# Performance work log

Measured on AMD Instinct MI355X. Metric: run time of the kernel, lower is better.

## Reference

```python
import jax, jax.numpy as jnp
import numpy as np

DIM = 512
HEADS = 8
SCALE = DIM ** (-0.5)  # scale_with_head=False


def setup_inputs() -> dict:
    key = jax.random.key(0)
    k1, k2, k3 = jax.random.split(key, 3)
    x = jax.random.normal(k1, (16, 1024, DIM), dtype=jnp.float32)
    w_qkv = jax.random.normal(k2, (DIM, 3 * DIM), dtype=jnp.float32) * (DIM ** -0.5)
    w_out = jax.random.normal(k3, (DIM, DIM), dtype=jnp.float32) * (DIM ** -0.5)
    b_out = jnp.zeros((DIM,), dtype=jnp.float32)
    return {"x": x, "w_qkv": w_qkv, "w_out": w_out, "b_out": b_out}


def reference(x, w_qkv, w_out, b_out):
    b, n, _ = x.shape
    h = HEADS
    qkv = x @ w_qkv  # [b, n, 3*dim]
    q, k, v = jnp.split(qkv, 3, axis=-1)
    # b n (h d) -> b h n d
    reshape = lambda t: t.reshape(b, n, h, -1).transpose(0, 2, 1, 3)
    q, k, v = reshape(q), reshape(k), reshape(v)
    dots = jnp.einsum('bhid,bhjd->bhij', q, k) * SCALE  # [b,h,n,n]
    attn = jax.nn.softmax(dots, axis=-1)
    out = jnp.einsum('bhij,bhjd->bhid', attn, v)
    out = out.transpose(0, 2, 1, 3).reshape(b, n, h * (DIM // h))  # b n (h d)
    return out @ w_out + b_out
```

## Files before the change

kernel.cpp:

```cpp
#include <hip/hip_runtime.h>
#include <math.h>


#define QSCALE_ 0.06376541773f
#define RESCALE_THR_ 8.0f

typedef float f32x4 __attribute__((ext_vector_type(4)));
typedef __bf16 bf16x8 __attribute__((ext_vector_type(8)));

static __device__ __forceinline__ ushort bf_bits(float f) {
    unsigned u = __builtin_bit_cast(unsigned, f);
    u += 0x7fffu + ((u >> 16) & 1u);
    return (ushort)(u >> 16);
}
static __device__ __forceinline__ unsigned cvt_pk_bf16(float lo, float hi) {
    unsigned d;
    asm("v_cvt_pk_bf16_f32 %0, %1, %2" : "=v"(d) : "v"(lo), "v"(hi));
    return d;
}

#define GLDS16(gsrc, ldst)                                                              \
    __builtin_amdgcn_global_load_lds((const __attribute__((address_space(1))) void*)(gsrc), \
                                     (__attribute__((address_space(3))) void*)(ldst), 16, 0, 0)

__global__ __launch_bounds__(256) void cast_bf16(const float* __restrict__ in,
                                                 ushort* __restrict__ out, int n4) {
    const int i = blockIdx.x * 256 + threadIdx.x;
    if (i >= n4) return;
    const float4 v = ((const float4*)in)[i];
    ushort4 o;
    o.x = bf_bits(v.x); o.y = bf_bits(v.y); o.z = bf_bits(v.z); o.w = bf_bits(v.w);
    ((ushort4*)out)[i] = o;
}

__global__ __launch_bounds__(256) void transpose_cast(const float* __restrict__ in,
                                                      ushort* __restrict__ out,
                                                      int K, int N, float scale, int scaleRows) {
    __shared__ float t[32][33];
    const int n0 = blockIdx.x * 32, k0 = blockIdx.y * 32;
    const int tx = threadIdx.x & 31, ty = threadIdx.x >> 5;
    for (int i = ty; i < 32; i += 8)
        t[i][tx] = in[(size_t)(k0 + i) * N + n0 + tx];
    __syncthreads();
    for (int i = ty; i < 32; i += 8) {
        const float s = (n0 + i < scaleRows) ? scale : 1.f;
        out[(size_t)(n0 + i) * K + k0 + tx] = bf_bits(t[tx][i] * s);
    }
}

__global__ __launch_bounds__(256) void gemm_bf16(const ushort* __restrict__ A,
                                                 const ushort* __restrict__ BT,
                                                 const float* __restrict__ bias,
                                                 float* __restrict__ C,
                                                 ushort* __restrict__ Cb,
                                                 ushort* __restrict__ VT,
                                                 int M, int N, int K) {
    __shared__ __align__(16) char lds[16384];
    const int tid = threadIdx.x;
    const int lane = tid & 63;
    const int w = tid >> 6;
    const int wr = w >> 1, wc = w & 1;
    const int fr = lane & 15;
    const int fg = lane >> 4;
    const int rowBase = blockIdx.y * 128;
    const int colBase = blockIdx.x * 128;

    f32x4 acc[4][4] = {};

    for (int k0 = 0; k0 < K; k0 += 32) {
#pragma unroll
        for (int r = 0; r < 2; ++r) {
            const unsigned boff = r * 4096u + w * 1024u + lane * 16u;
            const unsigned row = boff >> 6;
            const unsigned ke = (boff & 63u) >> 1;
            GLDS16(A + (size_t)(rowBase + row) * K + k0 + ke, lds + r * 4096 + w * 1024);
            GLDS16(BT + (size_t)(colBase + row) * K + k0 + ke, lds + 8192 + r * 4096 + w * 1024);
        }
        __syncthreads();

        bf16x8 a_frag[4], b_frag[4];
#pragma unroll
        for (int mi = 0; mi < 4; ++mi)
            a_frag[mi] = *(const bf16x8*)(lds + ((wr * 64 + mi * 16 + fr) * 64 + fg * 16));
#pragma unroll
        for (int ni = 0; ni < 4; ++ni)
            b_frag[ni] = *(const bf16x8*)(lds + 8192 + ((wc * 64 + ni * 16 + fr) * 64 + fg * 16));
#pragma unroll
        for (int mi = 0; mi < 4; ++mi)
#pragma unroll
            for (int ni = 0; ni < 4; ++ni)
                acc[mi][ni] = __builtin_amdgcn_mfma_f32_16x16x32_bf16(a_frag[mi], b_frag[ni],
                                                                      acc[mi][ni], 0, 0, 0);
        __syncthreads();
    }

#pragma unroll
    for (int ni = 0; ni < 4; ++ni) {
        const int col = colBase + wc * 64 + ni * 16 + fr;
        const float bv = bias ? bias[col] : 0.f;
#pragma unroll
        for (int mi = 0; mi < 4; ++mi) {
            const int row0 = rowBase + wr * 64 + mi * 16 + fg * 4;
            if (Cb) {
                if (VT && col >= 1024) {
                    const int hd = col - 1024;
                    const size_t vb = ((size_t)((row0 >> 10) * 8 + (hd >> 6)) * 64 + (hd & 63)) * 1024
                                      + (row0 & 1023);
                    ushort4 pk4;
                    pk4.x = bf_bits(acc[mi][ni][0]);
                    pk4.y = bf_bits(acc[mi][ni][1]);
                    pk4.z = bf_bits(acc[mi][ni][2]);
                    pk4.w = bf_bits(acc[mi][ni][3]);
                    *(ushort4*)(VT + vb) = pk4;
                } else {
#pragma unroll
                    for (int q = 0; q < 4; ++q)
                        Cb[(size_t)(row0 + q) * N + col] = bf_bits(acc[mi][ni][q]);
                }
            } else {
#pragma unroll
                for (int q = 0; q < 4; ++q)
                    C[(size_t)(row0 + q) * N + col] = acc[mi][ni][q] + bv;
            }
        }
    }
}

__global__ __launch_bounds__(256) void attn_mfma(const ushort* __restrict__ qkv,
                                                 const ushort* __restrict__ vT,
                                                 ushort* __restrict__ aoutb) {
    __shared__ __align__(16) char lds[40960];
    const int qt = blockIdx.x;
    const int bh = blockIdx.y;
    const int b = bh >> 3, h = bh & 7;
    const int tid = threadIdx.x;
    const int lane = tid & 63;
    const int w = tid >> 6;
    const int fr = lane & 15;
    const int fg = lane >> 4;

    const size_t nbase = (size_t)b * 1024;
    const int qrow0 = qt * 64;

    bf16x8 qf[2];
    {
        const size_t qa = (nbase + qrow0 + w * 16 + fr) * 1536 + h * 64;
        qf[0] = *(const bf16x8*)(qkv + qa + fg * 8);
        qf[1] = *(const bf16x8*)(qkv + qa + 32 + fg * 8);
    }

    const int srow = w * 16 + (lane >> 3);
    const int slot = lane & 7;
    auto stage = [&](int kt, int buf) {
        char* kd = lds + buf * 8192;
        char* vd = lds + 16384 + buf * 8192;
#pragma unroll
        for (int r = 0; r < 2; ++r) {
            const int row = srow + r * 8;
            const int sw = slot ^ (row & 7);
            GLDS16(qkv + (nbase + kt * 64 + row) * 1536 + 512 + h * 64 + sw * 8,
                   kd + (w * 2 + r) * 1024);
            GLDS16(vT + ((size_t)bh * 64 + row) * 1024 + kt * 64 + sw * 8,
                   vd + (w * 2 + r) * 1024);
        }
    };

    f32x4 o[4] = {};
    float mrow = -INFINITY, lrow = 0.f;

    stage(0, 0);
    __syncthreads();
    int cur = 0;
    char* const pbase = lds + 32768 + w * 2048;

    for (int kt = 0; kt < 16; ++kt) {
        if (kt < 15) stage(kt + 1, cur ^ 1);
        const char* kb = lds + cur * 8192;
        const char* vb = lds + 16384 + cur * 8192;

        f32x4 S[4];
#pragma unroll
        for (int jb = 0; jb < 4; ++jb) {
            f32x4 a = {};
#pragma unroll
            for (int s = 0; s < 2; ++s) {
                const int row = jb * 16 + fr;
                const int c = s * 64 + fg * 16;
                const bf16x8 kf = *(const bf16x8*)(kb + row * 128 + (c ^ ((row & 7) << 4)));
                a = __builtin_amdgcn_mfma_f32_16x16x32_bf16(kf, qf[s], a, 0, 0, 0);
            }
            S[jb] = a;
        }

        float tmax = -INFINITY;
#pragma unroll
        for (int jb = 0; jb < 4; ++jb)
#pragma unroll
            for (int r = 0; r < 4; ++r) tmax = fmaxf(tmax, S[jb][r]);
        tmax = fmaxf(tmax, __shfl_xor(tmax, 16));
        tmax = fmaxf(tmax, __shfl_xor(tmax, 32));

        if (!__all(tmax - mrow <= RESCALE_THR_)) {
            const float mnew = fmaxf(mrow, tmax);
            const float corr = __builtin_amdgcn_exp2f(mrow - mnew);
            mrow = mnew;
            lrow *= corr;
#pragma unroll
            for (int r = 0; r < 4; ++r) {
                const float cr = __shfl(corr, fg * 4 + r);
#pragma unroll
                for (int dvb = 0; dvb < 4; ++dvb) o[dvb][r] *= cr;
            }
        }

        float psum = 0.f;
#pragma unroll
        for (int jb = 0; jb < 4; ++jb)
#pragma unroll
            for (int r = 0; r < 4; ++r) {
                const float p = __builtin_amdgcn_exp2f(S[jb][r] - mrow);
                S[jb][r] = p;
                psum += p;
            }
        psum += __shfl_xor(psum, 16);
        psum += __shfl_xor(psum, 32);
        lrow += psum;

#pragma unroll
        for (int jb = 0; jb < 4; ++jb) {
            unsigned pk2[2];
            pk2[0] = cvt_pk_bf16(S[jb][0], S[jb][1]);
            pk2[1] = cvt_pk_bf16(S[jb][2], S[jb][3]);
            *(ulong1*)(pbase + fr * 128 + ((jb * 32 + fg * 8) ^ ((fr & 7) << 4))) =
                *(ulong1*)pk2;
        }

#pragma unroll
        for (int s = 0; s < 2; ++s) {
            const int pc = s * 64 + fg * 16;
            const bf16x8 pf = *(const bf16x8*)(pbase + fr * 128 + (pc ^ ((fr & 7) << 4)));
#pragma unroll
            for (int dvb = 0; dvb < 4; ++dvb) {
                const int vrow = dvb * 16 + fr;
                const bf16x8 vf = *(const bf16x8*)(vb + vrow * 128 + (pc ^ ((vrow & 7) << 4)));
                o[dvb] = __builtin_amdgcn_mfma_f32_16x16x32_bf16(pf, vf, o[dvb], 0, 0, 0);
            }
        }
        __syncthreads();
        cur ^= 1;
    }

#pragma unroll
    for (int r = 0; r < 4; ++r) {
        const float linv = 1.f / __shfl(lrow, fg * 4 + r);
        const size_t n = nbase + qrow0 + w * 16 + fg * 4 + r;
#pragma unroll
        for (int dvb = 0; dvb < 4; ++dvb)
            aoutb[n * 512 + h * 64 + dvb * 16 + fr] = bf_bits(o[dvb][r] * linv);
    }
}

extern "C" void kernel_launch(void* const* d_in, const int* in_sizes, int n_in,
                              void* d_out, int out_size, void* d_ws, size_t ws_size,
                              hipStream_t stream) {
    const float* x     = (const float*)d_in[0];
    const float* w_qkv = (const float*)d_in[1];
    const float* w_out = (const float*)d_in[2];
    const float* b_out = (const float*)d_in[3];
    float* out = (float*)d_out;

    char* ws = (char*)d_ws;
    ushort* qkvb  = (ushort*)ws;
    ushort* vT    = (ushort*)(ws + 50331648);
    ushort* xb    = (ushort*)(ws + 50331648 + 16777216);
    ushort* aoutb = xb;
    ushort* wqkvT = (ushort*)(ws + 50331648 + 33554432);
    ushort* woutT = (ushort*)(ws + 50331648 + 33554432 + 1572864);

    const dim3 blk(256);
    cast_bf16<<<dim3(8388608 / 4 / 256), blk, 0, stream>>>(x, xb, 8388608 / 4);
    transpose_cast<<<dim3(1536 / 32, 512 / 32), blk, 0, stream>>>(w_qkv, wqkvT, 512, 1536,
                                                                  QSCALE_, 512);
    transpose_cast<<<dim3(512 / 32, 512 / 32), blk, 0, stream>>>(w_out, woutT, 512, 512,
                                                                 1.f, 0);
    gemm_bf16<<<dim3(12, 128), blk, 0, stream>>>(xb, wqkvT, nullptr, nullptr, qkvb, vT,
                                                 16384, 1536, 512);
    attn_mfma<<<dim3(16, 128), blk, 0, stream>>>(qkvb, vT, aoutb);
    gemm_bf16<<<dim3(4, 128), blk, 0, stream>>>(aoutb, woutT, b_out, out, nullptr, nullptr,
                                                16384, 512, 512);
}
```

Before: 152.0 us.

## Fuse x cast into QKV GEMM and offload softmax row-sum to MFMA

Removes the standalone fp32-to-bf16 cast kernel for x. The QKV GEMM now loads fp32 rows directly, converts them in registers and writes them into a padded LDS tile. In the attention kernel, the row-sum of probabilities is computed by an MFMA against a ones vector instead of VALU adds and shuffles, and exp is fused into the bf16 packing. The kernel also adds s_setprio around MFMA blocks, uses 3-input max, and unrolls the K loop by two to fix buffer indices. The cost is that the fused GEMM re-reads fp32 x once per column block (12x) and swaps the async LDS loads for synchronous register loads.

```diff
diff --git a/kernel.cpp b/kernel.cpp
--- a/kernel.cpp
+++ b/kernel.cpp
@@ -18,20 +18,13 @@
     asm("v_cvt_pk_bf16_f32 %0, %1, %2" : "=v"(d) : "v"(lo), "v"(hi));
     return d;
 }
+static __device__ __forceinline__ float fmax3_(float a, float b, float c) {
+    return fmaxf(fmaxf(a, b), c);
+}
 
 #define GLDS16(gsrc, ldst)                                                              \
     __builtin_amdgcn_global_load_lds((const __attribute__((address_space(1))) void*)(gsrc), \
                                      (__attribute__((address_space(3))) void*)(ldst), 16, 0, 0)
-
-__global__ __launch_bounds__(256) void cast_bf16(const float* __restrict__ in,
-                                                 ushort* __restrict__ out, int n4) {
-    const int i = blockIdx.x * 256 + threadIdx.x;
-    if (i >= n4) return;
-    const float4 v = ((const float4*)in)[i];
-    ushort4 o;
-    o.x = bf_bits(v.x); o.y = bf_bits(v.y); o.z = bf_bits(v.z); o.w = bf_bits(v.w);
-    ((ushort4*)out)[i] = o;
-}
 
 __global__ __launch_bounds__(256) void transpose_cast(const float* __restrict__ in,
                                                       ushort* __restrict__ out,
@@ -48,14 +41,18 @@
     }
 }
 
-__global__ __launch_bounds__(256) void gemm_bf16(const ushort* __restrict__ A,
+template <bool FUSEA>
+__global__ __launch_bounds__(256) void gemm_bf16(const float* __restrict__ Af32,
+                                                 const ushort* __restrict__ A,
                                                  const ushort* __restrict__ BT,
                                                  const float* __restrict__ bias,
                                                  float* __restrict__ C,
                                                  ushort* __restrict__ Cb,
                                                  ushort* __restrict__ VT,
                                                  int M, int N, int K) {
-    __shared__ __align__(16) char lds[16384];
+    constexpr int ASTR = FUSEA ? 80 : 64;
+    constexpr int BOFF = FUSEA ? 10240 : 8192;
+    __shared__ __align__(16) char lds[BOFF + 8192];
     const int tid = threadIdx.x;
     const int lane = tid & 63;
     const int w = tid >> 6;
@@ -68,23 +65,47 @@
     f32x4 acc[4][4] = {};
 
     for (int k0 = 0; k0 < K; k0 += 32) {
-#pragma unroll
-        for (int r = 0; r < 2; ++r) {
-            const unsigned boff = r * 4096u + w * 1024u + lane * 16u;
-            const unsigned row = boff >> 6;
-            const unsigned ke = (boff & 63u) >> 1;
-            GLDS16(A + (size_t)(rowBase + row) * K + k0 + ke, lds + r * 4096 + w * 1024);
-            GLDS16(BT + (size_t)(colBase + row) * K + k0 + ke, lds + 8192 + r * 4096 + w * 1024);
+        if constexpr (FUSEA) {
+            const int ar = tid >> 1, kh = tid & 1;
+            const float* src = Af32 + (size_t)(rowBase + ar) * K + k0 + kh * 16;
+            const float4 v0 = ((const float4*)src)[0];
+            const float4 v1 = ((const float4*)src)[1];
+            const float4 v2 = ((const float4*)src)[2];
+            const float4 v3 = ((const float4*)src)[3];
+            uint4 lo, hi;
+            lo.x = cvt_pk_bf16(v0.x, v0.y); lo.y = cvt_pk_bf16(v0.z, v0.w);
+            lo.z = cvt_pk_bf16(v1.x, v1.y); lo.w = cvt_pk_bf16(v1.z, v1.w);
+            hi.x = cvt_pk_bf16(v2.x, v2.y); hi.y = cvt_pk_bf16(v2.z, v2.w);
+            hi.z = cvt_pk_bf16(v3.x, v3.y); hi.w = cvt_pk_bf16(v3.z, v3.w);
+            char* dst = lds + ar * 80 + kh * 32;
+            *(uint4*)dst = lo;
+            *(uint4*)(dst + 16) = hi;
+#pragma unroll
+            for (int r = 0; r < 2; ++r) {
+                const unsigned boff = r * 4096u + w * 1024u + lane * 16u;
+                const unsigned row = boff >> 6;
+                const unsigned ke = (boff & 63u) >> 1;
+                GLDS16(BT + (size_t)(colBase + row) * K + k0 + ke, lds + BOFF + r * 4096 + w * 1024);
+            }
+        } else {
+#pragma unroll
+            for (int r = 0; r < 2; ++r) {
+                const unsigned boff = r * 4096u + w * 1024u + lane * 16u;
+                const unsigned row = boff >> 6;
+                const unsigned ke = (boff & 63u) >> 1;
+                GLDS16(A + (size_t)(rowBase + row) * K + k0 + ke, lds + r * 4096 + w * 1024);
+                GLDS16(BT + (size_t)(colBase + row) * K + k0 + ke, lds + BOFF + r * 4096 + w * 1024);
+            }
         }
         __syncthreads();
 
         bf16x8 a_frag[4], b_frag[4];
 #pragma unroll
         for (int mi = 0; mi < 4; ++mi)
-            a_frag[mi] = *(const bf16x8*)(lds + ((wr * 64 + mi * 16 + fr) * 64 + fg * 16));
+            a_frag[mi] = *(const bf16x8*)(lds + (wr * 64 + mi * 16 + fr) * ASTR + fg * 16);
 #pragma unroll
         for (int ni = 0; ni < 4; ++ni)
-            b_frag[ni] = *(const bf16x8*)(lds + 8192 + ((wc * 64 + ni * 16 + fr) * 64 + fg * 16));
+            b_frag[ni] = *(const bf16x8*)(lds + BOFF + (wc * 64 + ni * 16 + fr) * 64 + fg * 16);
 #pragma unroll
         for (int mi = 0; mi < 4; ++mi)
 #pragma unroll
@@ -149,6 +170,10 @@
         qf[1] = *(const bf16x8*)(qkv + qa + 32 + fg * 8);
     }
 
+    bf16x8 onesf;
+#pragma unroll
+    for (int e = 0; e < 8; ++e) onesf[e] = __builtin_bit_cast(__bf16, (ushort)0x3F80);
+
     const int srow = w * 16 + (lane >> 3);
     const int slot = lane & 7;
     auto stage = [&](int kt, int buf) {
@@ -166,19 +191,20 @@
     };
 
     f32x4 o[4] = {};
-    float mrow = -INFINITY, lrow = 0.f;
+    f32x4 lacc = {};
+    float mrow = -INFINITY;
 
     stage(0, 0);
     __syncthreads();
-    int cur = 0;
     char* const pbase = lds + 32768 + w * 2048;
 
-    for (int kt = 0; kt < 16; ++kt) {
+    auto tile = [&](int kt, int cur) {
         if (kt < 15) stage(kt + 1, cur ^ 1);
         const char* kb = lds + cur * 8192;
         const char* vb = lds + 16384 + cur * 8192;
 
         f32x4 S[4];
+        __builtin_amdgcn_s_setprio(1);
 #pragma unroll
         for (int jb = 0; jb < 4; ++jb) {
             f32x4 a = {};
@@ -191,12 +217,16 @@
             }
             S[jb] = a;
         }
-
-        float tmax = -INFINITY;
-#pragma unroll
-        for (int jb = 0; jb < 4; ++jb)
-#pragma unroll
-            for (int r = 0; r < 4; ++r) tmax = fmaxf(tmax, S[jb][r]);
+        __builtin_amdgcn_s_setprio(0);
+
+        float tmax = fmax3_(S[0][0], S[0][1], S[0][2]);
+        tmax = fmax3_(tmax, S[0][3], S[1][0]);
+        tmax = fmax3_(tmax, S[1][1], S[1][2]);
+        tmax = fmax3_(tmax, S[1][3], S[2][0]);
+        tmax = fmax3_(tmax, S[2][1], S[2][2]);
+        tmax = fmax3_(tmax, S[2][3], S[3][0]);
+        tmax = fmax3_(tmax, S[3][1], S[3][2]);
+        tmax = fmaxf(tmax, S[3][3]);
         tmax = fmaxf(tmax, __shfl_xor(tmax, 16));
         tmax = fmaxf(tmax, __shfl_xor(tmax, 32));
 
@@ -204,41 +234,32 @@
             const float mnew = fmaxf(mrow, tmax);
             const float corr = __builtin_amdgcn_exp2f(mrow - mnew);
             mrow = mnew;
-            lrow *= corr;
 #pragma unroll
             for (int r = 0; r < 4; ++r) {
                 const float cr = __shfl(corr, fg * 4 + r);
+                lacc[r] *= cr;
 #pragma unroll
                 for (int dvb = 0; dvb < 4; ++dvb) o[dvb][r] *= cr;
             }
         }
-
-        float psum = 0.f;
-#pragma unroll
-        for (int jb = 0; jb < 4; ++jb)
-#pragma unroll
-            for (int r = 0; r < 4; ++r) {
-                const float p = __builtin_amdgcn_exp2f(S[jb][r] - mrow);
-                S[jb][r] = p;
-                psum += p;
-            }
-        psum += __shfl_xor(psum, 16);
-        psum += __shfl_xor(psum, 32);
-        lrow += psum;
 
 #pragma unroll
         for (int jb = 0; jb < 4; ++jb) {
             unsigned pk2[2];
-            pk2[0] = cvt_pk_bf16(S[jb][0], S[jb][1]);
-            pk2[1] = cvt_pk_bf16(S[jb][2], S[jb][3]);
+            pk2[0] = cvt_pk_bf16(__builtin_amdgcn_exp2f(S[jb][0] - mrow),
+                                 __builtin_amdgcn_exp2f(S[jb][1] - mrow));
+            pk2[1] = cvt_pk_bf16(__builtin_amdgcn_exp2f(S[jb][2] - mrow),
+                                 __builtin_amdgcn_exp2f(S[jb][3] - mrow));
             *(ulong1*)(pbase + fr * 128 + ((jb * 32 + fg * 8) ^ ((fr & 7) << 4))) =
                 *(ulong1*)pk2;
         }
 
+        __builtin_amdgcn_s_setprio(1);
 #pragma unroll
         for (int s = 0; s < 2; ++s) {
             const int pc = s * 64 + fg * 16;
             const bf16x8 pf = *(const bf16x8*)(pbase + fr * 128 + (pc ^ ((fr & 7) << 4)));
+            lacc = __builtin_amdgcn_mfma_f32_16x16x32_bf16(pf, onesf, lacc, 0, 0, 0);
 #pragma unroll
             for (int dvb = 0; dvb < 4; ++dvb) {
                 const int vrow = dvb * 16 + fr;
@@ -246,13 +267,18 @@
                 o[dvb] = __builtin_amdgcn_mfma_f32_16x16x32_bf16(pf, vf, o[dvb], 0, 0, 0);
             }
         }
+        __builtin_amdgcn_s_setprio(0);
         __syncthreads();
-        cur ^= 1;
+    };
+
+    for (int kt = 0; kt < 16; kt += 2) {
+        tile(kt, 0);
+        tile(kt + 1, 1);
     }
 
 #pragma unroll
     for (int r = 0; r < 4; ++r) {
-        const float linv = 1.f / __shfl(lrow, fg * 4 + r);
+        const float linv = 1.f / lacc[r];
         const size_t n = nbase + qrow0 + w * 16 + fg * 4 + r;
 #pragma unroll
         for (int dvb = 0; dvb < 4; ++dvb)
@@ -272,20 +298,18 @@
     char* ws = (char*)d_ws;
     ushort* qkvb  = (ushort*)ws;
     ushort* vT    = (ushort*)(ws + 50331648);
-    ushort* xb    = (ushort*)(ws + 50331648 + 16777216);
-    ushort* aoutb = xb;
+    ushort* aoutb = (ushort*)(ws + 50331648 + 16777216);
     ushort* wqkvT = (ushort*)(ws + 50331648 + 33554432);
     ushort* woutT = (ushort*)(ws + 50331648 + 33554432 + 1572864);
 
     const dim3 blk(256);
-    cast_bf16<<<dim3(8388608 / 4 / 256), blk, 0, stream>>>(x, xb, 8388608 / 4);
     transpose_cast<<<dim3(1536 / 32, 512 / 32), blk, 0, stream>>>(w_qkv, wqkvT, 512, 1536,
                                                                   QSCALE_, 512);
     transpose_cast<<<dim3(512 / 32, 512 / 32), blk, 0, stream>>>(w_out, woutT, 512, 512,
                                                                  1.f, 0);
-    gemm_bf16<<<dim3(12, 128), blk, 0, stream>>>(xb, wqkvT, nullptr, nullptr, qkvb, vT,
-                                                 16384, 1536, 512);
+    gemm_bf16<true><<<dim3(12, 128), blk, 0, stream>>>(x, nullptr, wqkvT, nullptr,
+                                                       nullptr, qkvb, vT, 16384, 1536, 512);
     attn_mfma<<<dim3(16, 128), blk, 0, stream>>>(qkvb, vT, aoutb);
-    gemm_bf16<<<dim3(4, 128), blk, 0, stream>>>(aoutb, woutT, b_out, out, nullptr, nullptr,
-                                                16384, 512, 512);
-}
+    gemm_bf16<false><<<dim3(4, 128), blk, 0, stream>>>(nullptr, aoutb, woutT, b_out,
+                                                       out, nullptr, nullptr, 16384, 512, 512);
+}
```

Result: slower. 160.9 us (+5.9%).
